# Kernel optimization log

Measured on AMD Instinct MI355X. Metric: run time of the kernel, lower is better.

## Reference

```python
import jax, jax.numpy as jnp
import numpy as np
import itertools

B, RES, RES_, STRIDE = 256, 14, 7, 2
N, N_ = RES * RES, RES_ * RES_
IN_DIM, OUT_DIM = 384, 512
H, KD, AR = 12, 32, 2
D = AR * KD            # 64, per-head value dim
DH = D * H             # 768
NH_KD = KD * H         # 384
KV_H = DH + NH_KD      # 1152
EPS = 1e-5


def _bias_idxs():
    # Replicates the relative-offset indexing from __init__.
    points = list(itertools.product(range(RES), range(RES)))
    points_ = list(itertools.product(range(RES_), range(RES_)))
    offsets, idxs = {}, []
    for p1 in points_:
        for p2 in points:
            off = (abs(p1[0] * STRIDE - p2[0]), abs(p1[1] * STRIDE - p2[1]))
            if off not in offsets:
                offsets[off] = len(offsets)
            idxs.append(offsets[off])
    return np.array(idxs, dtype=np.int32).reshape(N_, N), len(offsets)


def linear_bn(x, w, gamma, beta, mean, var):
    # Linear (no bias) followed by BatchNorm1d in inference form (fused affine).
    s = gamma / jnp.sqrt(var + EPS)
    return jnp.matmul(x, w.T) * s + (beta - mean * s)


def setup_inputs() -> dict:
    key = jax.random.key(0)
    ks = jax.random.split(key, 12)
    idxs_np, n_off = _bias_idxs()

    def bn_params(k, dim):
        k1, k2, k3, k4 = jax.random.split(k, 4)
        return (jax.random.normal(k1, (dim,)) * 0.1 + 1.0,   # gamma
                jax.random.normal(k2, (dim,)) * 0.1,          # beta
                jax.random.normal(k3, (dim,)) * 0.1,          # running_mean
                jax.random.uniform(k4, (dim,), minval=0.5, maxval=1.5))  # running_var

    kv_g, kv_b, kv_m, kv_v = bn_params(ks[1], KV_H)
    q_g, q_b, q_m, q_v = bn_params(ks[3], NH_KD)
    pr_g, pr_b, pr_m, pr_v = bn_params(ks[5], OUT_DIM)

    return {
        "x": jax.random.normal(ks[0], (B, N, IN_DIM), dtype=jnp.float32),
        "kv_w": jax.random.normal(ks[6], (KV_H, IN_DIM), dtype=jnp.float32) * (IN_DIM ** -0.5),
        "kv_g": kv_g, "kv_b": kv_b, "kv_m": kv_m, "kv_v": kv_v,
        "q_w": jax.random.normal(ks[7], (NH_KD, IN_DIM), dtype=jnp.float32) * (IN_DIM ** -0.5),
        "q_g": q_g, "q_b": q_b, "q_m": q_m, "q_v": q_v,
        "proj_w": jax.random.normal(ks[8], (OUT_DIM, DH), dtype=jnp.float32) * (DH ** -0.5),
        "proj_g": pr_g, "proj_b": pr_b, "proj_m": pr_m, "proj_v": pr_v,
        "attention_biases": jax.random.normal(ks[9], (H, n_off), dtype=jnp.float32) * 0.02,
        "bias_idxs": jnp.asarray(idxs_np),
    }


def reference(x, kv_w, kv_g, kv_b, kv_m, kv_v,
              q_w, q_g, q_b, q_m, q_v,
              proj_w, proj_g, proj_b, proj_m, proj_v,
              attention_biases, bias_idxs):
    Bsz = x.shape[0]
    scale = KD ** -0.5
    # kv projection: [B, N, H, KD+D] -> split into k, v
    kv = linear_bn(x, kv_w, kv_g, kv_b, kv_m, kv_v).reshape(Bsz, N, H, KD + D)
    k, v = kv[..., :KD], kv[..., KD:]
    # strided subsample of queries: [B, 14, 14, C] -> [B, 49, C]
    xs = x.reshape(Bsz, RES, RES, IN_DIM)[:, ::STRIDE, ::STRIDE].reshape(Bsz, N_, IN_DIM)
    q = linear_bn(xs, q_w, q_g, q_b, q_m, q_v).reshape(Bsz, N_, H, KD)
    # attention with gathered relative-position bias: bias [H, N_, N]
    bias = attention_biases[:, bias_idxs]
    attn = jnp.einsum('bqhd,bkhd->bhqk', q, k) * scale + bias
    attn = jax.nn.softmax(attn, axis=-1)
    out = jnp.einsum('bhqk,bkhd->bqhd', attn, v).reshape(Bsz, N_, DH)
    out = jax.nn.hard_swish(out)
    return linear_bn(out, proj_w, proj_g, proj_b, proj_m, proj_v)
```

## Files before the change

### kernel.cpp

```cpp
#include <hip/hip_runtime.h>
#include <hip/hip_bf16.h>
#include <math.h>

typedef unsigned short U16;
typedef unsigned int U32;
typedef __attribute__((ext_vector_type(8))) short bf8;
typedef __attribute__((ext_vector_type(4))) float f4;
typedef __attribute__((ext_vector_type(4))) unsigned short u16x4;

#define AS1 __attribute__((address_space(1)))
#define AS3 __attribute__((address_space(3)))

#define BSZ   256
#define NTOK  196
#define NQ    49
#define INDIM 384
#define OUTD  512
#define NH    12
#define DV    64
#define DHD   768
#define KVH   1152
#define NPADR 224

__device__ inline U16 f2bf(float f){
    __hip_bfloat16 h = __float2bfloat16(f);
    return *(U16*)&h;
}
__device__ inline f4 f4zero(){ f4 z; z[0]=0.f; z[1]=0.f; z[2]=0.f; z[3]=0.f; return z; }
__device__ inline bf8 bf8zero(){ bf8 v;
#pragma unroll
    for (int j=0;j<8;++j) v[j]=0; return v; }

__global__ void k_cast8p(const float* __restrict__ in, U16* __restrict__ out, int n8){
    int i = blockIdx.x*256 + threadIdx.x;
    if (i >= n8) return;
    int rall = i / 48;
    int c8   = i - rall*48;
    int b    = rall / NPADR;
    int r    = rall - b*NPADR;
    U16 o[8];
    if (r < NTOK){
        const float* p = in + ((size_t)(b*NTOK + r))*INDIM + c8*8;
#pragma unroll
        for (int j=0;j<8;++j) o[j] = f2bf(p[j]);
    } else {
#pragma unroll
        for (int j=0;j<8;++j) o[j] = 0;
    }
    *(bf8*)(out + (size_t)i*8) = *(const bf8*)o;
}

__global__ void k_castxs(const float* __restrict__ x, U16* __restrict__ out, int n8){
    int i = blockIdx.x*256 + threadIdx.x;
    if (i >= n8) return;
    int row = i / 48;
    int c8  = i - row*48;
    int b   = row / 49;
    int q   = row - b*49;
    int r_  = q / 7, c_ = q - r_*7;
    const float* p = x + ((size_t)(b*NTOK + 28*r_ + 2*c_))*INDIM + c8*8;
    U16 o[8];
#pragma unroll
    for (int j=0;j<8;++j) o[j] = f2bf(p[j]);
    *(bf8*)(out + (size_t)i*8) = *(const bf8*)o;
}

#define W1C (KVH*INDIM/8)
#define W2C (INDIM*INDIM/8)
#define W3C (OUTD*DHD/8)
__global__ void k_castw(const float* __restrict__ w1, const float* __restrict__ w2,
                        const float* __restrict__ w3, U16* __restrict__ o1,
                        U16* __restrict__ o2, U16* __restrict__ o3){
    int i = blockIdx.x*256 + threadIdx.x;
    const float* p; U16* o;
    if (i < W1C){ p = w1 + (size_t)i*8; o = o1 + (size_t)i*8; }
    else if (i < W1C+W2C){ int k=i-W1C; p = w2 + (size_t)k*8; o = o2 + (size_t)k*8; }
    else if (i < W1C+W2C+W3C){ int k=i-W1C-W2C; p = w3 + (size_t)k*8; o = o3 + (size_t)k*8; }
    else return;
    U16 t[8];
#pragma unroll
    for (int j=0;j<8;++j) t[j] = f2bf(p[j]);
    *(bf8*)o = *(const bf8*)t;
}

#define BIAS_N   (NH*NQ*NTOK)
#define BIAS_BLK ((BIAS_N+255)/256)
#define BN_BLK   ((KVH+INDIM+OUTD)/256)
__global__ void k_misc(const float* __restrict__ ab, const int* __restrict__ idxs, int n_off,
                       const float* __restrict__ g1, const float* __restrict__ b1,
                       const float* __restrict__ m1, const float* __restrict__ v1,
                       const float* __restrict__ g2, const float* __restrict__ b2,
                       const float* __restrict__ m2, const float* __restrict__ v2,
                       const float* __restrict__ g3, const float* __restrict__ b3,
                       const float* __restrict__ m3, const float* __restrict__ v3,
                       float* __restrict__ s1, float* __restrict__ bo1,
                       float* __restrict__ s2, float* __restrict__ bo2,
                       float* __restrict__ s3, float* __restrict__ bo3,
                       float* __restrict__ bias_out){
    int blk = blockIdx.x;
    int tid = threadIdx.x;
    if (blk < BIAS_BLK){
        int i = blk*256 + tid;
        if (i < BIAS_N){
            int h = i / (NQ*NTOK);
            int qk = i - h*(NQ*NTOK);
            bias_out[i] = ab[h*n_off + idxs[qk]];
        }
    } else {
        int i = (blk-BIAS_BLK)*256 + tid;
        const float *g,*b,*m,*v; float *so,*bo; int k;
        if (i < KVH){ g=g1;b=b1;m=m1;v=v1;so=s1;bo=bo1;k=i; }
        else if (i < KVH+INDIM){ g=g2;b=b2;m=m2;v=v2;so=s2;bo=bo2;k=i-KVH; }
        else { g=g3;b=b3;m=m3;v=v3;so=s3;bo=bo3;k=i-KVH-INDIM; }
        float s = g[k] / sqrtf(v[k] + 1e-5f);
        so[k] = s;
        bo[k] = b[k] - m[k]*s;
    }
}

#define FA1 14336
#define FB0 28672
#define FB1 34816
#define VL  7168
#define PL  21504
__global__ __launch_bounds__(256,2) void k_fused(
    const U16* __restrict__ xbf, const U16* __restrict__ kvw, const U16* __restrict__ qo_,
    const float* __restrict__ skv, const float* __restrict__ bkv,
    const float* __restrict__ biasf, U16* __restrict__ aout)
{
    __shared__ U16 smem[40960];
    const int hw = blockIdx.x;
    const int bh = (hw & 7)*384 + (hw >> 3);
    const int b = bh / NH, h = bh - b*NH;
    const int tid = threadIdx.x, lane = tid & 63, w = tid >> 6;
    const int wm = w & 1, wn = w >> 1;
    const int l15 = lane & 15, oct = lane >> 4;

    U16* Ab[2] = { smem + 0,   smem + FA1 };
    U16* Bb[2] = { smem + FB0, smem + FB1 };

    U32 aoff[7];
#pragma unroll
    for (int c=0;c<7;++c){
        int s = c*256 + tid;
        int ach = s / NPADR, ar = s - ach*NPADR;
        aoff[c] = (U32)(b*NPADR + ar)*INDIM + ach*8;
    }
    U32 boff[3];
#pragma unroll
    for (int c=0;c<3;++c){
        int s = c*256 + tid;
        int bch = s / 96, br = s - bch*96;
        boff[c] = (U32)(h*96 + br)*INDIM + bch*8;
    }

    f4 acc[7][3];
#pragma unroll
    for (int i=0;i<7;++i)
#pragma unroll
        for (int j=0;j<3;++j) acc[i][j] = f4zero();

#define STAGE(buf, kb) do{ \
    _Pragma("unroll") \
    for (int c=0;c<7;++c) \
        __builtin_amdgcn_global_load_lds((const AS1 U32*)(xbf + aoff[c] + (kb)), \
            (AS3 U32*)(Ab[buf] + (c*256+tid)*8), 16, 0, 0); \
    _Pragma("unroll") \
    for (int c=0;c<3;++c) \
        __builtin_amdgcn_global_load_lds((const AS1 U32*)(kvw + boff[c] + (kb)), \
            (AS3 U32*)(Bb[buf] + (c*256+tid)*8), 16, 0, 0); \
}while(0)

    STAGE(0, 0);

#pragma unroll
    for (int kt=0; kt<6; ++kt){
        const int cur = kt & 1;
        if (kt < 5){
            STAGE(cur^1, (kt+1)*64);
            asm volatile("s_waitcnt vmcnt(10)" ::: "memory");
        } else {
            asm volatile("s_waitcnt vmcnt(0)" ::: "memory");
        }
        __builtin_amdgcn_sched_barrier(0);
        __builtin_amdgcn_s_barrier();
        __builtin_amdgcn_sched_barrier(0);

#pragma unroll
        for (int kk=0;kk<2;++kk){
            bf8 af[7], bfr[3];
#pragma unroll
            for (int i=0;i<7;++i)
                af[i]  = *(const bf8*)(Ab[cur] + ((kk*4+oct)*NPADR + wm*112 + i*16 + l15)*8);
#pragma unroll
            for (int j=0;j<3;++j)
                bfr[j] = *(const bf8*)(Bb[cur] + ((kk*4+oct)*96 + wn*48 + j*16 + l15)*8);
            __builtin_amdgcn_s_setprio(1);
#pragma unroll
            for (int i=0;i<7;++i)
#pragma unroll
                for (int j=0;j<3;++j)
                    acc[i][j] = __builtin_amdgcn_mfma_f32_16x16x32_bf16(af[i], bfr[j], acc[i][j], 0, 0, 0);
            __builtin_amdgcn_s_setprio(0);
        }
        __builtin_amdgcn_sched_barrier(0);
        __builtin_amdgcn_s_barrier();
        __builtin_amdgcn_sched_barrier(0);
    }
#undef STAGE

#pragma unroll
    for (int j=0;j<3;++j){
        const int cc = wn*48 + j*16 + l15;
        const float sc = skv[h*96 + cc];
        const float bi = bkv[h*96 + cc];
#pragma unroll
        for (int i=0;i<7;++i){
            const int n0 = wm*112 + i*16 + oct*4;
            if (cc < 32){
#pragma unroll
                for (int r=0;r<4;++r)
                    smem[((cc>>3)*NPADR + n0 + r)*8 + (cc&7)] = f2bf(acc[i][j][r]*sc + bi);
            } else {
                const int dv = cc - 32;
                u16x4 pk;
#pragma unroll
                for (int r=0;r<4;++r) pk[r] = f2bf(acc[i][j][r]*sc + bi);
                *(u16x4*)(smem + VL + ((n0>>3)*64 + dv)*8 + (oct&1)*4) = pk;
            }
        }
    }
    __syncthreads();

    const int qg = w*16 + l15;
    bf8 qf = bf8zero();
    if (qg < NQ) qf = *(const bf8*)(qo_ + ((size_t)(b*NQ + qg))*INDIM + h*32 + oct*8);

    f4 sacc[14];
#pragma unroll
    for (int mt=0;mt<14;++mt) sacc[mt] = f4zero();
#pragma unroll
    for (int mt=0;mt<14;++mt){
        const bf8 kf = *(const bf8*)(smem + (oct*NPADR + mt*16 + l15)*8);
        sacc[mt] = __builtin_amdgcn_mfma_f32_16x16x32_bf16(kf, qf, sacc[mt], 0, 0, 0);
    }

    const float scale = 0.17677669529663689f;
    float mx = -1e30f;
#pragma unroll
    for (int mt=0;mt<14;++mt){
        const int n0 = mt*16 + oct*4;
        f4 bi4 = f4zero();
        if (qg < NQ && n0 < NTOK) bi4 = *(const f4*)(biasf + ((size_t)h*NQ + qg)*NTOK + n0);
#pragma unroll
        for (int r=0;r<4;++r){
            float s = (n0 + r < NTOK) ? sacc[mt][r]*scale + bi4[r] : -1e30f;
            sacc[mt][r] = s;
            mx = fmaxf(mx, s);
        }
    }
    mx = fmaxf(mx, __shfl_xor(mx, 16));
    mx = fmaxf(mx, __shfl_xor(mx, 32));

    float sum = 0.f;
#pragma unroll
    for (int mt=0;mt<14;++mt){
#pragma unroll
        for (int r=0;r<4;++r){
            float p = (mt*16 + oct*4 + r < NTOK) ? __expf(sacc[mt][r] - mx) : 0.f;
            sacc[mt][r] = p;
            sum += p;
        }
    }
    sum += __shfl_xor(sum, 16);
    sum += __shfl_xor(sum, 32);
    const float inv = 1.f / sum;

    const int prow = w*16 + l15;
    const int pbase = PL + prow*NPADR;
    const int psw = prow & 3;
#pragma unroll
    for (int mt=0;mt<14;++mt){
        u16x4 pk;
#pragma unroll
        for (int r=0;r<4;++r) pk[r] = f2bf(sacc[mt][r]*inv);
        const int blk = (mt*2 + (oct>>1)) ^ psw;
        *(u16x4*)(smem + pbase + blk*8 + (oct&1)*4) = pk;
    }

    f4 pacc[4];
#pragma unroll
    for (int dt=0;dt<4;++dt) pacc[dt] = f4zero();
#pragma unroll
    for (int kt=0;kt<7;++kt){
        const bf8 pa = *(const bf8*)(smem + pbase + ((kt*4 + oct) ^ psw)*8);
#pragma unroll
        for (int dt=0;dt<4;++dt){
            const bf8 vf = *(const bf8*)(smem + VL + ((kt*4 + oct)*64 + dt*16 + l15)*8);
            pacc[dt] = __builtin_amdgcn_mfma_f32_16x16x32_bf16(pa, vf, pacc[dt], 0, 0, 0);
        }
    }

#pragma unroll
    for (int dt=0;dt<4;++dt){
#pragma unroll
        for (int r=0;r<4;++r){
            const int qo2 = w*16 + oct*4 + r;
            if (qo2 < NQ){
                const int d = dt*16 + l15;
                float v = pacc[dt][r];
                float tt = fminf(fmaxf(v + 3.f, 0.f), 6.f);
                aout[((size_t)(b*NQ + qo2))*DHD + h*DV + d] = f2bf(v * tt * (1.f/6.f));
            }
        }
    }
}

__global__ __launch_bounds__(256,2) void k_qgemm(
    const U16* __restrict__ A, const U16* __restrict__ Bw,
    const float* __restrict__ s_arr, const float* __restrict__ b_arr,
    U16* __restrict__ o16)
{
    __shared__ U16 smem[32768];
    U16* Ab[2] = { smem,          smem + 8192 };
    U16* Bb[2] = { smem + 16384,  smem + 24576 };
    const int gn0 = blockIdx.x * 128;
    const int gm0 = blockIdx.y * 128;
    const int tid  = threadIdx.x;
    const int lane = tid & 63;
    const int w    = tid >> 6;
    const int wm   = w >> 1, wn = w & 1;
    const int l15  = lane & 15, oct = lane >> 4;

    f4 acc[4][4];
#pragma unroll
    for (int i=0;i<4;++i)
#pragma unroll
        for (int j=0;j<4;++j) acc[i][j] = f4zero();

    size_t aoff[4], boff[4];
#pragma unroll
    for (int c=0;c<4;++c){
        int slot = c*256 + tid;
        int row = slot & 127, ch = slot >> 7;
        aoff[c] = (size_t)(gm0 + row)*INDIM + ch*8;
        boff[c] = (size_t)(gn0 + row)*INDIM + ch*8;
    }

#pragma unroll
    for (int c=0;c<4;++c){
        __builtin_amdgcn_global_load_lds((const AS1 U32*)(A + aoff[c]),
            (AS3 U32*)(Ab[0] + (c*256+tid)*8), 16, 0, 0);
        __builtin_amdgcn_global_load_lds((const AS1 U32*)(Bw + boff[c]),
            (AS3 U32*)(Bb[0] + (c*256+tid)*8), 16, 0, 0);
    }

#pragma unroll
    for (int kt=0; kt<6; ++kt){
        const int cur = kt & 1;
        if (kt+1 < 6){
            const int kb = (kt+1)*64;
#pragma unroll
            for (int c=0;c<4;++c){
                __builtin_amdgcn_global_load_lds((const AS1 U32*)(A + aoff[c] + kb),
                    (AS3 U32*)(Ab[cur^1] + (c*256+tid)*8), 16, 0, 0);
                __builtin_amdgcn_global_load_lds((const AS1 U32*)(Bw + boff[c] + kb),
                    (AS3 U32*)(Bb[cur^1] + (c*256+tid)*8), 16, 0, 0);
            }
            asm volatile("s_waitcnt vmcnt(8)" ::: "memory");
        } else {
            asm volatile("s_waitcnt vmcnt(0)" ::: "memory");
        }
        __builtin_amdgcn_sched_barrier(0);
        __builtin_amdgcn_s_barrier();
        __builtin_amdgcn_sched_barrier(0);

#pragma unroll
        for (int kk=0;kk<2;++kk){
            bf8 af[4], bfr[4];
#pragma unroll
            for (int i=0;i<4;++i)
                af[i]  = *(const bf8*)(Ab[cur] + ((kk*4+oct)*128 + wm*64 + i*16 + l15)*8);
#pragma unroll
            for (int j=0;j<4;++j)
                bfr[j] = *(const bf8*)(Bb[cur] + ((kk*4+oct)*128 + wn*64 + j*16 + l15)*8);
            __builtin_amdgcn_s_setprio(1);
#pragma unroll
            for (int i=0;i<4;++i)
#pragma unroll
                for (int j=0;j<4;++j)
                    acc[i][j] = __builtin_amdgcn_mfma_f32_16x16x32_bf16(af[i], bfr[j], acc[i][j], 0, 0, 0);
            __builtin_amdgcn_s_setprio(0);
        }
        __builtin_amdgcn_sched_barrier(0);
        __builtin_amdgcn_s_barrier();
        __builtin_amdgcn_sched_barrier(0);
    }

#pragma unroll
    for (int j=0;j<4;++j){
        const int col = gn0 + wn*64 + j*16 + l15;
        const float sc = s_arr[col];
        const float bi = b_arr[col];
#pragma unroll
        for (int i=0;i<4;++i){
            const int row0 = gm0 + wm*64 + i*16 + oct*4;
#pragma unroll
            for (int r=0;r<4;++r)
                o16[(size_t)(row0+r)*INDIM + col] = f2bf(acc[i][j][r]*sc + bi);
        }
    }
}

__global__ __launch_bounds__(256,2) void k_proj(
    const U16* __restrict__ A, const U16* __restrict__ Bw,
    const float* __restrict__ s_arr, const float* __restrict__ b_arr,
    float* __restrict__ o32)
{
    __shared__ U16 smem[32768];
    U16* Ab[2] = { smem,          smem + 8192 };
    U16* Bb[2] = { smem + 16384,  smem + 24576 };
    const int l   = (blockIdx.x & 7)*49 + (blockIdx.x >> 3);
    const int gn0 = (l & 3) * 128;
    const int gm0 = (l >> 2) * 128;
    const int tid  = threadIdx.x;
    const int lane = tid & 63;
    const int w    = tid >> 6;
    const int wm   = w >> 1, wn = w & 1;
    const int l15  = lane & 15, oct = lane >> 4;

    f4 acc[4][4];
#pragma unroll
    for (int i=0;i<4;++i)
#pragma unroll
        for (int j=0;j<4;++j) acc[i][j] = f4zero();

    size_t aoff[4], boff[4];
#pragma unroll
    for (int c=0;c<4;++c){
        int slot = c*256 + tid;
        int row = slot & 127, ch = slot >> 7;
        aoff[c] = (size_t)(gm0 + row)*DHD + ch*8;
        boff[c] = (size_t)(gn0 + row)*DHD + ch*8;
    }

#pragma unroll
    for (int c=0;c<4;++c){
        __builtin_amdgcn_global_load_lds((const AS1 U32*)(A + aoff[c]),
            (AS3 U32*)(Ab[0] + (c*256+tid)*8), 16, 0, 0);
        __builtin_amdgcn_global_load_lds((const AS1 U32*)(Bw + boff[c]),
            (AS3 U32*)(Bb[0] + (c*256+tid)*8), 16, 0, 0);
    }

#pragma unroll
    for (int kt=0; kt<12; ++kt){
        const int cur = kt & 1;
        if (kt+1 < 12){
            const int kb = (kt+1)*64;
#pragma unroll
            for (int c=0;c<4;++c){
                __builtin_amdgcn_global_load_lds((const AS1 U32*)(A + aoff[c] + kb),
                    (AS3 U32*)(Ab[cur^1] + (c*256+tid)*8), 16, 0, 0);
                __builtin_amdgcn_global_load_lds((const AS1 U32*)(Bw + boff[c] + kb),
                    (AS3 U32*)(Bb[cur^1] + (c*256+tid)*8), 16, 0, 0);
            }
            asm volatile("s_waitcnt vmcnt(8)" ::: "memory");
        } else {
            asm volatile("s_waitcnt vmcnt(0)" ::: "memory");
        }
        __builtin_amdgcn_sched_barrier(0);
        __builtin_amdgcn_s_barrier();
        __builtin_amdgcn_sched_barrier(0);

#pragma unroll
        for (int kk=0;kk<2;++kk){
            bf8 af[4], bfr[4];
#pragma unroll
            for (int i=0;i<4;++i)
                af[i]  = *(const bf8*)(Ab[cur] + ((kk*4+oct)*128 + wm*64 + i*16 + l15)*8);
#pragma unroll
            for (int j=0;j<4;++j)
                bfr[j] = *(const bf8*)(Bb[cur] + ((kk*4+oct)*128 + wn*64 + j*16 + l15)*8);
            __builtin_amdgcn_s_setprio(1);
#pragma unroll
            for (int i=0;i<4;++i)
#pragma unroll
                for (int j=0;j<4;++j)
                    acc[i][j] = __builtin_amdgcn_mfma_f32_16x16x32_bf16(af[i], bfr[j], acc[i][j], 0, 0, 0);
            __builtin_amdgcn_s_setprio(0);
        }
        __builtin_amdgcn_sched_barrier(0);
        __builtin_amdgcn_s_barrier();
        __builtin_amdgcn_sched_barrier(0);
    }

#pragma unroll
    for (int j=0;j<4;++j){
        const int col = gn0 + wn*64 + j*16 + l15;
        const float sc = s_arr[col];
        const float bi = b_arr[col];
#pragma unroll
        for (int i=0;i<4;++i){
            const int row0 = gm0 + wm*64 + i*16 + oct*4;
#pragma unroll
            for (int r=0;r<4;++r)
                o32[(size_t)(row0+r)*OUTD + col] = acc[i][j][r]*sc + bi;
        }
    }
}

extern "C" void kernel_launch(void* const* d_in, const int* in_sizes, int n_in,
                              void* d_out, int out_size, void* d_ws, size_t ws_size,
                              hipStream_t stream)
{
    const float* x    = (const float*)d_in[0];
    const float* kv_w = (const float*)d_in[1];
    const float* kv_g = (const float*)d_in[2];
    const float* kv_b = (const float*)d_in[3];
    const float* kv_m = (const float*)d_in[4];
    const float* kv_v = (const float*)d_in[5];
    const float* q_w  = (const float*)d_in[6];
    const float* q_g  = (const float*)d_in[7];
    const float* q_b  = (const float*)d_in[8];
    const float* q_m  = (const float*)d_in[9];
    const float* q_v  = (const float*)d_in[10];
    const float* pr_w = (const float*)d_in[11];
    const float* pr_g = (const float*)d_in[12];
    const float* pr_b = (const float*)d_in[13];
    const float* pr_m = (const float*)d_in[14];
    const float* pr_v = (const float*)d_in[15];
    const float* ab   = (const float*)d_in[16];
    const int*  idxs  = (const int*)d_in[17];
    const int n_off = in_sizes[16] / NH;

    char* ws = (char*)d_ws;
    size_t off = 0;
    auto alloc = [&](size_t bytes)->char*{
        char* p = ws + off; off += (bytes + 255) & ~(size_t)255; return p;
    };
    U16*   x_bf   = (U16*)  alloc((size_t)BSZ*NPADR*INDIM*2);
    U16*   xs_bf  = (U16*)  alloc((size_t)BSZ*NQ*INDIM*2);
    U16*   kvw_bf = (U16*)  alloc((size_t)KVH*INDIM*2);
    U16*   qw_bf  = (U16*)  alloc((size_t)INDIM*INDIM*2);
    U16*   prw_bf = (U16*)  alloc((size_t)OUTD*DHD*2);
    float* s_kv   = (float*)alloc(KVH*4);
    float* b_kv   = (float*)alloc(KVH*4);
    float* s_q    = (float*)alloc(INDIM*4);
    float* b_q    = (float*)alloc(INDIM*4);
    float* s_pr   = (float*)alloc(OUTD*4);
    float* b_pr   = (float*)alloc(OUTD*4);
    float* biasf  = (float*)alloc(((size_t)NH*NQ*NTOK + 256)*4);
    U16*   q_out  = (U16*)  alloc((size_t)BSZ*NQ*INDIM*2);
    U16*   a_out  = (U16*)  alloc((size_t)BSZ*NQ*DHD*2);
    if (off > ws_size) return;

    {
        int n8 = BSZ*NPADR*INDIM/8;
        k_cast8p<<<(n8+255)/256, 256, 0, stream>>>(x, x_bf, n8);
    }
    {
        int n8 = BSZ*NQ*INDIM/8;
        k_castxs<<<(n8+255)/256, 256, 0, stream>>>(x, xs_bf, n8);
    }
    k_castw<<<(W1C+W2C+W3C+255)/256, 256, 0, stream>>>(kv_w, q_w, pr_w, kvw_bf, qw_bf, prw_bf);
    k_misc<<<BIAS_BLK+BN_BLK, 256, 0, stream>>>(
        ab, idxs, n_off,
        kv_g, kv_b, kv_m, kv_v, q_g, q_b, q_m, q_v, pr_g, pr_b, pr_m, pr_v,
        s_kv, b_kv, s_q, b_q, s_pr, b_pr, biasf);

    {
        dim3 g(INDIM/128, BSZ*NQ/128);
        k_qgemm<<<g, 256, 0, stream>>>(xs_bf, qw_bf, s_q, b_q, q_out);
    }
    k_fused<<<BSZ*NH, 256, 0, stream>>>(x_bf, kvw_bf, q_out, s_kv, b_kv, biasf, a_out);
    k_proj<<<392, 256, 0, stream>>>(a_out, prw_bf, s_pr, b_pr, (float*)d_out);
}
```

Measured before the change: 197.1 us.

## Halve LDS footprint to raise occupancy, pass P via shuffles instead of LDS

Shrinks the fused attention kernel's shared memory from 80KB to 40KB by halving the K-tile (32 instead of 64, 12 iterations instead of 6) and overlapping the K/V staging regions with the GEMM buffers. The launch bound goes from 2 to 4 blocks per CU. The softmax probabilities are now moved into MFMA A-operand layout with cross-lane shuffles instead of an LDS round trip, and V storage is truncated to rows below 200. In exchange there are more barriers per K, finer-grained loads, and extra shuffle work, and register pressure under the new launch bound may force spills.

```diff
diff --git a/kernel.cpp b/kernel.cpp
--- a/kernel.cpp
+++ b/kernel.cpp
@@ -118,17 +118,13 @@
     }
 }
 
-#define FA1 14336
-#define FB0 28672
-#define FB1 34816
-#define VL  7168
-#define PL  21504
-__global__ __launch_bounds__(256,2) void k_fused(
+#define KLO 12800
+__global__ __launch_bounds__(256,4) void k_fused(
     const U16* __restrict__ xbf, const U16* __restrict__ kvw, const U16* __restrict__ qo_,
     const float* __restrict__ skv, const float* __restrict__ bkv,
     const float* __restrict__ biasf, U16* __restrict__ aout)
 {
-    __shared__ U16 smem[40960];
+    __shared__ U16 smem[20480];
     const int hw = blockIdx.x;
     const int bh = (hw & 7)*384 + (hw >> 3);
     const int b = bh / NH, h = bh - b*NH;
@@ -136,22 +132,29 @@
     const int wm = w & 1, wn = w >> 1;
     const int l15 = lane & 15, oct = lane >> 4;
 
-    U16* Ab[2] = { smem + 0,   smem + FA1 };
-    U16* Bb[2] = { smem + FB0, smem + FB1 };
-
-    U32 aoff[7];
-#pragma unroll
-    for (int c=0;c<7;++c){
+    U16* Ab[2] = { smem + 0,     smem + 7168 };
+    U16* Bb[2] = { smem + 14336, smem + 17408 };
+
+    U32 aoff[4];
+#pragma unroll
+    for (int c=0;c<3;++c){
         int s = c*256 + tid;
         int ach = s / NPADR, ar = s - ach*NPADR;
         aoff[c] = (U32)(b*NPADR + ar)*INDIM + ach*8;
     }
-    U32 boff[3];
-#pragma unroll
-    for (int c=0;c<3;++c){
-        int s = c*256 + tid;
-        int bch = s / 96, br = s - bch*96;
-        boff[c] = (U32)(h*96 + br)*INDIM + bch*8;
+    {
+        int s = 768 + (tid & 127);
+        int ach = s / NPADR, ar = s - ach*NPADR;
+        aoff[3] = (U32)(b*NPADR + ar)*INDIM + ach*8;
+    }
+    U32 boff[2];
+    {
+        int s0 = tid;
+        int bc0 = s0 / 96, br0 = s0 - bc0*96;
+        boff[0] = (U32)(h*96 + br0)*INDIM + bc0*8;
+        int s1 = 128 + (tid | 128);
+        int bc1 = s1 / 96, br1 = s1 - bc1*96;
+        boff[1] = (U32)(h*96 + br1)*INDIM + bc1*8;
     }
 
     f4 acc[7][3];
@@ -162,23 +165,27 @@
 
 #define STAGE(buf, kb) do{ \
     _Pragma("unroll") \
-    for (int c=0;c<7;++c) \
+    for (int c=0;c<3;++c) \
         __builtin_amdgcn_global_load_lds((const AS1 U32*)(xbf + aoff[c] + (kb)), \
             (AS3 U32*)(Ab[buf] + (c*256+tid)*8), 16, 0, 0); \
-    _Pragma("unroll") \
-    for (int c=0;c<3;++c) \
-        __builtin_amdgcn_global_load_lds((const AS1 U32*)(kvw + boff[c] + (kb)), \
-            (AS3 U32*)(Bb[buf] + (c*256+tid)*8), 16, 0, 0); \
+    if (tid < 128) \
+        __builtin_amdgcn_global_load_lds((const AS1 U32*)(xbf + aoff[3] + (kb)), \
+            (AS3 U32*)(Ab[buf] + (768+tid)*8), 16, 0, 0); \
+    __builtin_amdgcn_global_load_lds((const AS1 U32*)(kvw + boff[0] + (kb)), \
+        (AS3 U32*)(Bb[buf] + tid*8), 16, 0, 0); \
+    if (tid >= 128) \
+        __builtin_amdgcn_global_load_lds((const AS1 U32*)(kvw + boff[1] + (kb)), \
+            (AS3 U32*)(Bb[buf] + (128+tid)*8), 16, 0, 0); \
 }while(0)
 
     STAGE(0, 0);
 
 #pragma unroll
-    for (int kt=0; kt<6; ++kt){
+    for (int kt=0; kt<12; ++kt){
         const int cur = kt & 1;
-        if (kt < 5){
-            STAGE(cur^1, (kt+1)*64);
-            asm volatile("s_waitcnt vmcnt(10)" ::: "memory");
+        if (kt < 11){
+            STAGE(cur^1, (kt+1)*32);
+            asm volatile("s_waitcnt vmcnt(5)" ::: "memory");
         } else {
             asm volatile("s_waitcnt vmcnt(0)" ::: "memory");
         }
@@ -186,23 +193,20 @@
         __builtin_amdgcn_s_barrier();
         __builtin_amdgcn_sched_barrier(0);
 
-#pragma unroll
-        for (int kk=0;kk<2;++kk){
-            bf8 af[7], bfr[3];
-#pragma unroll
-            for (int i=0;i<7;++i)
-                af[i]  = *(const bf8*)(Ab[cur] + ((kk*4+oct)*NPADR + wm*112 + i*16 + l15)*8);
+        bf8 af[7], bfr[3];
+#pragma unroll
+        for (int i=0;i<7;++i)
+            af[i]  = *(const bf8*)(Ab[cur] + (oct*NPADR + wm*112 + i*16 + l15)*8);
+#pragma unroll
+        for (int j=0;j<3;++j)
+            bfr[j] = *(const bf8*)(Bb[cur] + (oct*96 + wn*48 + j*16 + l15)*8);
+        __builtin_amdgcn_s_setprio(1);
+#pragma unroll
+        for (int i=0;i<7;++i)
 #pragma unroll
             for (int j=0;j<3;++j)
-                bfr[j] = *(const bf8*)(Bb[cur] + ((kk*4+oct)*96 + wn*48 + j*16 + l15)*8);
-            __builtin_amdgcn_s_setprio(1);
-#pragma unroll
-            for (int i=0;i<7;++i)
-#pragma unroll
-                for (int j=0;j<3;++j)
-                    acc[i][j] = __builtin_amdgcn_mfma_f32_16x16x32_bf16(af[i], bfr[j], acc[i][j], 0, 0, 0);
-            __builtin_amdgcn_s_setprio(0);
-        }
+                acc[i][j] = __builtin_amdgcn_mfma_f32_16x16x32_bf16(af[i], bfr[j], acc[i][j], 0, 0, 0);
+        __builtin_amdgcn_s_setprio(0);
         __builtin_amdgcn_sched_barrier(0);
         __builtin_amdgcn_s_barrier();
         __builtin_amdgcn_sched_barrier(0);
@@ -220,13 +224,13 @@
             if (cc < 32){
 #pragma unroll
                 for (int r=0;r<4;++r)
-                    smem[((cc>>3)*NPADR + n0 + r)*8 + (cc&7)] = f2bf(acc[i][j][r]*sc + bi);
-            } else {
+                    smem[KLO + ((cc>>3)*NPADR + n0 + r)*8 + (cc&7)] = f2bf(acc[i][j][r]*sc + bi);
+            } else if (n0 < 200){
                 const int dv = cc - 32;
                 u16x4 pk;
 #pragma unroll
                 for (int r=0;r<4;++r) pk[r] = f2bf(acc[i][j][r]*sc + bi);
-                *(u16x4*)(smem + VL + ((n0>>3)*64 + dv)*8 + (oct&1)*4) = pk;
+                *(u16x4*)(smem + ((n0>>3)*64 + dv)*8 + (oct&1)*4) = pk;
             }
         }
     }
@@ -241,7 +245,7 @@
     for (int mt=0;mt<14;++mt) sacc[mt] = f4zero();
 #pragma unroll
     for (int mt=0;mt<14;++mt){
-        const bf8 kf = *(const bf8*)(smem + (oct*NPADR + mt*16 + l15)*8);
+        const bf8 kf = *(const bf8*)(smem + KLO + (oct*NPADR + mt*16 + l15)*8);
         sacc[mt] = __builtin_amdgcn_mfma_f32_16x16x32_bf16(kf, qf, sacc[mt], 0, 0, 0);
     }
 
@@ -276,28 +280,34 @@
     sum += __shfl_xor(sum, 32);
     const float inv = 1.f / sum;
 
-    const int prow = w*16 + l15;
-    const int pbase = PL + prow*NPADR;
-    const int psw = prow & 3;
+    U32 pw0[14], pw1[14];
 #pragma unroll
     for (int mt=0;mt<14;++mt){
-        u16x4 pk;
-#pragma unroll
-        for (int r=0;r<4;++r) pk[r] = f2bf(sacc[mt][r]*inv);
-        const int blk = (mt*2 + (oct>>1)) ^ psw;
-        *(u16x4*)(smem + pbase + blk*8 + (oct&1)*4) = pk;
-    }
-
+        pw0[mt] = (U32)f2bf(sacc[mt][0]*inv) | ((U32)f2bf(sacc[mt][1]*inv) << 16);
+        pw1[mt] = (U32)f2bf(sacc[mt][2]*inv) | ((U32)f2bf(sacc[mt][3]*inv) << 16);
+    }
+
+    const int src1 = l15 + (oct & 1)*32;
+    const int src2 = src1 + 16;
+    const bool hiT = (oct >> 1) != 0;
     f4 pacc[4];
 #pragma unroll
     for (int dt=0;dt<4;++dt) pacc[dt] = f4zero();
 #pragma unroll
     for (int kt=0;kt<7;++kt){
-        const bf8 pa = *(const bf8*)(smem + pbase + ((kt*4 + oct) ^ psw)*8);
+        U32 a0 = __shfl(pw0[2*kt],   src1), a1 = __shfl(pw1[2*kt],   src1);
+        U32 c0 = __shfl(pw0[2*kt+1], src1), c1 = __shfl(pw1[2*kt+1], src1);
+        U32 b0 = __shfl(pw0[2*kt],   src2), b1 = __shfl(pw1[2*kt],   src2);
+        U32 d0 = __shfl(pw0[2*kt+1], src2), d1 = __shfl(pw1[2*kt+1], src2);
+        union { U32 u[4]; bf8 v; } pu;
+        pu.u[0] = hiT ? c0 : a0;
+        pu.u[1] = hiT ? c1 : a1;
+        pu.u[2] = hiT ? d0 : b0;
+        pu.u[3] = hiT ? d1 : b1;
 #pragma unroll
         for (int dt=0;dt<4;++dt){
-            const bf8 vf = *(const bf8*)(smem + VL + ((kt*4 + oct)*64 + dt*16 + l15)*8);
-            pacc[dt] = __builtin_amdgcn_mfma_f32_16x16x32_bf16(pa, vf, pacc[dt], 0, 0, 0);
+            const bf8 vf = *(const bf8*)(smem + ((kt*4 + oct)*64 + dt*16 + l15)*8);
+            pacc[dt] = __builtin_amdgcn_mfma_f32_16x16x32_bf16(pu.v, vf, pacc[dt], 0, 0, 0);
         }
     }
 
```

Result: slower. 345.4 us (+75.2%).
